# Kernel optimization log

Hardware: AMD Instinct MI355X
Metric: run time of the kernel (lower is better)

## Reference

```python
import jax, jax.numpy as jnp
import numpy as np
import math

B, T, C, H = 2, 2048, 512, 8
TOPK = 64
HD = C // H
EPS = 1e-12  # torch F.normalize eps


def setup_inputs() -> dict:
    key = jax.random.key(0)
    ks = jax.random.split(key, 6)
    s = 1.0 / math.sqrt(C)
    q = jax.random.normal(ks[0], (B, T, C), dtype=jnp.float32)
    tgt_mask = jnp.tril(jnp.ones((T, T), dtype=jnp.float32)).reshape(1, 1, T, T)
    Wq = jax.random.normal(ks[1], (C, C), dtype=jnp.float32) * s
    Wk = jax.random.normal(ks[2], (C, C), dtype=jnp.float32) * s
    Wv = jax.random.normal(ks[3], (C, C), dtype=jnp.float32) * s
    Wp = jax.random.normal(ks[4], (C, C), dtype=jnp.float32) * s
    bq = jnp.zeros((C,), jnp.float32)
    bk = jnp.zeros((C,), jnp.float32)
    bv = jnp.zeros((C,), jnp.float32)
    bp = jnp.zeros((C,), jnp.float32)
    return {"q": q, "tgt_mask": tgt_mask, "Wq": Wq, "bq": bq, "Wk": Wk, "bk": bk,
            "Wv": Wv, "bv": bv, "Wp": Wp, "bp": bp}


def _attn(q, tgt_mask, Wq, bq, Wk, bk, Wv, bv, Wp, bp):
    Bt, Tt, Ct = q.shape
    # self-attention: k = v = q (module path when k, v are None)
    qh = (q @ Wq + bq).reshape(Bt, Tt, H, HD).transpose(0, 2, 1, 3)  # [B,H,T,hd]
    kh = (q @ Wk + bk).reshape(Bt, Tt, H, HD).transpose(0, 2, 1, 3)
    vh = (q @ Wv + bv).reshape(Bt, Tt, H, HD).transpose(0, 2, 1, 3)
    # L2-normalize v along head dim (F.normalize, p=2, eps=1e-12)
    vn = jnp.linalg.norm(vh, axis=-1, keepdims=True)
    vh = vh / jnp.maximum(vn, EPS)
    att = jnp.einsum('bhqd,bhkd->bhqk', qh, kh) * (1.0 / math.sqrt(HD))
    neg = -jnp.inf
    att = jnp.where(tgt_mask[:, :, :Tt, :Tt] == 0, neg, att)
    # top-k sparsification: drop entries strictly below the k-th largest per row
    top = jax.lax.top_k(att, TOPK)[0]            # [B,H,T,TOPK]
    vk = top[..., -1:]                            # k-th largest threshold
    att = jnp.where(att < vk, neg, att)
    att = jax.nn.softmax(att, axis=-1)
    y = jnp.einsum('bhqk,bhkd->bhqd', att, vh)
    y = y.transpose(0, 2, 1, 3).reshape(Bt, Tt, Ct)
    return y @ Wp + bp


def reference(q, tgt_mask, Wq, bq, Wk, bk, Wv, bv, Wp, bp):
    return _attn(q, tgt_mask, Wq, bq, Wk, bk, Wv, bv, Wp, bp)
```

## Files before the change

kernel.cpp:

```cpp
#include <hip/hip_runtime.h>
#include <cstdint>
#include <math.h>

static constexpr int Bc = 2, Tc = 2048, Cch = 512, Hc = 8;
static constexpr int BT = Bc * Tc;
static constexpr int NBH = Bc * Hc;
static constexpr int NRT = Tc / 128;
static constexpr int NTRI = NRT * (NRT + 1) / 2;
static constexpr size_t TRI_FLOATS = (size_t)NTRI * 16384;

typedef float f32x4 __attribute__((ext_vector_type(4)));
typedef short s16x8 __attribute__((ext_vector_type(8)));
typedef unsigned short u16x8 __attribute__((ext_vector_type(8)));
typedef unsigned short u16x4 __attribute__((ext_vector_type(4)));

__device__ __host__ inline constexpr int tri_i(int r) { return r * (r + 1) / 2; }

__device__ inline float wave_sum_f(float x) {
#pragma unroll
  for (int o = 32; o; o >>= 1) x += __shfl_xor(x, o);
  return x;
}
__device__ inline unsigned short f2bf(float x) {
  unsigned u = __float_as_uint(x);
  return (unsigned short)((u + 0x7FFFu + ((u >> 16) & 1u)) >> 16);
}
__device__ inline float bf2f(unsigned short h) { return __uint_as_float(((unsigned)h) << 16); }
__device__ inline float su2f(unsigned s) {
  unsigned u = (s & 0x80000000u) ? (s ^ 0x80000000u) : ~s;
  return __uint_as_float(u);
}

__global__ __launch_bounds__(256) void split_k(const float* __restrict__ X,
    unsigned short* __restrict__ hi, unsigned short* __restrict__ lo, int n8) {
  int i = blockIdx.x * 256 + threadIdx.x;
  if (i >= n8) return;
  const f32x4* p = (const f32x4*)X + (size_t)i * 2;
  f32x4 a = p[0], b = p[1];
  float v[8] = {a[0], a[1], a[2], a[3], b[0], b[1], b[2], b[3]};
  u16x8 h, l;
#pragma unroll
  for (int c = 0; c < 8; c++) {
    unsigned short hh = f2bf(v[c]);
    h[c] = hh;
    l[c] = f2bf(v[c] - bf2f(hh));
  }
  *(u16x8*)(hi + (size_t)i * 8) = h;
  *(u16x8*)(lo + (size_t)i * 8) = l;
}

__global__ __launch_bounds__(256) void splitT_k(const float* __restrict__ W,
    unsigned short* __restrict__ hiT, unsigned short* __restrict__ loT) {
  __shared__ float t[64][65];
  const int tid = threadIdx.x;
  const int k0 = blockIdx.x * 64, n0 = blockIdx.y * 64;
#pragma unroll
  for (int p = 0; p < 4; p++) {
    int idx = tid + p * 256, kk = idx >> 4, n4 = idx & 15;
    f32x4 v = *(const f32x4*)&W[(size_t)(k0 + kk) * Cch + n0 + n4 * 4];
    t[kk][n4 * 4 + 0] = v[0]; t[kk][n4 * 4 + 1] = v[1];
    t[kk][n4 * 4 + 2] = v[2]; t[kk][n4 * 4 + 3] = v[3];
  }
  __syncthreads();
  {
    int n = tid >> 2, ks = tid & 3;
    u16x8 h0, h1, l0, l1;
#pragma unroll
    for (int kk = 0; kk < 8; kk++) {
      float x = t[ks * 16 + kk][n];
      unsigned short hh = f2bf(x);
      h0[kk] = hh; l0[kk] = f2bf(x - bf2f(hh));
      float y = t[ks * 16 + 8 + kk][n];
      unsigned short hy = f2bf(y);
      h1[kk] = hy; l1[kk] = f2bf(y - bf2f(hy));
    }
    size_t base = (size_t)(n0 + n) * Cch + k0 + ks * 16;
    *(u16x8*)(hiT + base) = h0; *(u16x8*)(hiT + base + 8) = h1;
    *(u16x8*)(loT + base) = l0; *(u16x8*)(loT + base + 8) = l1;
  }
}

template <int BF16OUT>
__global__ __launch_bounds__(256) void gemm3_k(
    const unsigned short* __restrict__ Ahi, const unsigned short* __restrict__ Alo,
    const unsigned short* __restrict__ Bhi, const unsigned short* __restrict__ Blo,
    const float* __restrict__ bias, void* __restrict__ Out) {
  __shared__ unsigned short Ah[2][64][72];
  __shared__ unsigned short Bs[2][64][72];
  const int tid = threadIdx.x;
  const int w = tid >> 6, lane = tid & 63, e = lane >> 4, lr = lane & 15;
  const int wr = w >> 1, wc = w & 1;
  const int brow = blockIdx.y * 64, bcol = blockIdx.x * 64;
  f32x4 acc[2][2] = {};
  for (int k0 = 0; k0 < Cch; k0 += 64) {
#pragma unroll
    for (int p = 0; p < 2; p++) {
      int idx = tid + p * 256, row = idx >> 3, seg = idx & 7;
      *(u16x8*)&Ah[0][row][seg * 8] = *(const u16x8*)&Ahi[(size_t)(brow + row) * Cch + k0 + seg * 8];
      *(u16x8*)&Ah[1][row][seg * 8] = *(const u16x8*)&Alo[(size_t)(brow + row) * Cch + k0 + seg * 8];
      *(u16x8*)&Bs[0][row][seg * 8] = *(const u16x8*)&Bhi[(size_t)(bcol + row) * Cch + k0 + seg * 8];
      *(u16x8*)&Bs[1][row][seg * 8] = *(const u16x8*)&Blo[(size_t)(bcol + row) * Cch + k0 + seg * 8];
    }
    __syncthreads();
#pragma unroll
    for (int ks = 0; ks < 2; ks++) {
      s16x8 ah[2], al[2], bh[2], bl[2];
#pragma unroll
      for (int ti = 0; ti < 2; ti++) {
        ah[ti] = *(const s16x8*)&Ah[0][wr * 32 + ti * 16 + lr][ks * 32 + e * 8];
        al[ti] = *(const s16x8*)&Ah[1][wr * 32 + ti * 16 + lr][ks * 32 + e * 8];
      }
#pragma unroll
      for (int tj = 0; tj < 2; tj++) {
        bh[tj] = *(const s16x8*)&Bs[0][wc * 32 + tj * 16 + lr][ks * 32 + e * 8];
        bl[tj] = *(const s16x8*)&Bs[1][wc * 32 + tj * 16 + lr][ks * 32 + e * 8];
      }
#pragma unroll
      for (int ti = 0; ti < 2; ti++)
#pragma unroll
        for (int tj = 0; tj < 2; tj++) {
          acc[ti][tj] = __builtin_amdgcn_mfma_f32_16x16x32_bf16(ah[ti], bh[tj], acc[ti][tj], 0, 0, 0);
          acc[ti][tj] = __builtin_amdgcn_mfma_f32_16x16x32_bf16(ah[ti], bl[tj], acc[ti][tj], 0, 0, 0);
          acc[ti][tj] = __builtin_amdgcn_mfma_f32_16x16x32_bf16(al[ti], bh[tj], acc[ti][tj], 0, 0, 0);
        }
    }
    __syncthreads();
  }
#pragma unroll
  for (int ti = 0; ti < 2; ti++)
#pragma unroll
    for (int tj = 0; tj < 2; tj++) {
      int col = bcol + wc * 32 + tj * 16 + lr;
      float bi = bias[col];
#pragma unroll
      for (int r = 0; r < 4; r++) {
        int row = brow + wr * 32 + ti * 16 + e * 4 + r;
        float v = acc[ti][tj][r] + bi;
        if (BF16OUT) ((unsigned short*)Out)[(size_t)row * Cch + col] = f2bf(v);
        else         ((float*)Out)[(size_t)row * Cch + col] = v;
      }
    }
}

__global__ __launch_bounds__(256) void vnormt_k(const float* __restrict__ Vf,
                                                unsigned short* __restrict__ Vt) {
  __shared__ unsigned short T[64][72];
  const int tid = threadIdx.x;
  const int t0 = blockIdx.x * 64;
  const int h = blockIdx.y;
  const int tok = tid >> 2;
  const int q = tid & 3;
  const float* src = Vf + (size_t)(t0 + tok) * Cch + h * 64 + q * 16;
  f32x4 v[4];
  float ss = 0.f;
#pragma unroll
  for (int i = 0; i < 4; i++) {
    v[i] = *(const f32x4*)(src + i * 4);
#pragma unroll
    for (int c = 0; c < 4; c++) ss += v[i][c] * v[i][c];
  }
  ss += __shfl_xor(ss, 1);
  ss += __shfl_xor(ss, 2);
  float inv = 1.0f / fmaxf(sqrtf(ss), 1e-12f);
#pragma unroll
  for (int i = 0; i < 4; i++)
#pragma unroll
    for (int c = 0; c < 4; c++)
      T[q * 16 + i * 4 + c][tok] = f2bf(v[i][c] * inv);
  __syncthreads();
  const int d = tid >> 2, s2 = (tid & 3) * 2;
  const int b = t0 >> 11;
  size_t base = ((size_t)((b * Hc + h) * 64 + d)) * Tc + (t0 & 2047);
  *(u16x8*)(Vt + base + s2 * 8)     = *(const u16x8*)&T[d][s2 * 8];
  *(u16x8*)(Vt + base + s2 * 8 + 8) = *(const u16x8*)&T[d][s2 * 8 + 8];
}

__global__ __launch_bounds__(512) void sqk_k(const unsigned short* __restrict__ Qp,
    const unsigned short* __restrict__ Kp, float* __restrict__ S, int bh0) {
  __shared__ unsigned short Qs[128][72], Ks[128][72];
  int rt, ct;
  {
    int i = blockIdx.x;
    int r = (int)((sqrtf(8.f * i + 1.f) - 1.f) * 0.5f);
    while ((r + 1) * (r + 2) / 2 <= i) r++;
    while (r * (r + 1) / 2 > i) r--;
    rt = r; ct = i - r * (r + 1) / 2;
  }
  const int bh = bh0 + blockIdx.y, b = bh >> 3, h = bh & 7;
  const int tid = threadIdx.x, w = tid >> 6, lane = tid & 63, e = lane >> 4, lr = lane & 15;
#pragma unroll
  for (int p = 0; p < 2; p++) {
    int idx = tid + p * 512, row = idx >> 3, seg = idx & 7;
    *(u16x8*)&Qs[row][seg * 8] = *(const u16x8*)&Qp[((size_t)(b * Tc + rt * 128 + row)) * Cch + h * 64 + seg * 8];
    *(u16x8*)&Ks[row][seg * 8] = *(const u16x8*)&Kp[((size_t)(b * Tc + ct * 128 + row)) * Cch + h * 64 + seg * 8];
  }
  __syncthreads();
  f32x4 acc[8] = {};
  s16x8 a[2];
#pragma unroll
  for (int ks = 0; ks < 2; ks++) a[ks] = *(const s16x8*)&Qs[w * 16 + lr][ks * 32 + e * 8];
#pragma unroll
  for (int tj = 0; tj < 8; tj++) {
#pragma unroll
    for (int ks = 0; ks < 2; ks++) {
      s16x8 bb = *(const s16x8*)&Ks[tj * 16 + lr][ks * 32 + e * 8];
      acc[tj] = __builtin_amdgcn_mfma_f32_16x16x32_bf16(a[ks], bb, acc[tj], 0, 0, 0);
    }
  }
  float* Srow0 = S + (size_t)(bh - bh0) * TRI_FLOATS + (size_t)tri_i(rt) * 16384;
  const int stride = (rt + 1) * 128;
#pragma unroll
  for (int tj = 0; tj < 8; tj++)
#pragma unroll
    for (int r = 0; r < 4; r++) {
      int row = w * 16 + e * 4 + r;
      Srow0[(size_t)row * stride + ct * 128 + tj * 16 + lr] = acc[tj][r] * 0.125f;
    }
}

__global__ __launch_bounds__(512) void sel_k(float* __restrict__ S) {
  int wid = blockIdx.x * 8 + (threadIdx.x >> 6);
  int lane = threadIdx.x & 63;
  int bhl = wid >> 11, t = wid & 2047;
  int rt = t >> 7, lrow = t & 127;
  int stride = (rt + 1) * 128;
  float* row = S + (size_t)bhl * TRI_FLOATS + (size_t)tri_i(rt) * 16384 + (size_t)lrow * stride;
  unsigned su[32];
#pragma unroll
  for (int c = 0; c < 8; c++) {
    if (c * 256 < stride) {
      int j0 = c * 256 + lane * 4;
      f32x4 v;
      if (j0 < stride) v = *(const f32x4*)(row + j0);
      else { v[0] = v[1] = v[2] = v[3] = -INFINITY; }
#pragma unroll
      for (int cc = 0; cc < 4; cc++) {
        float x = (j0 + cc <= t) ? v[cc] : -INFINITY;
        unsigned u = __float_as_uint(x);
        su[c * 4 + cc] = (u & 0x80000000u) ? ~u : (u | 0x80000000u);
      }
    } else {
#pragma unroll
      for (int cc = 0; cc < 4; cc++) su[c * 4 + cc] = 0x007FFFFFu;
    }
  }
  unsigned lo = 0;
#pragma unroll 1
  for (int bit = 31; bit >= 0; bit--) {
    unsigned cand = lo | (1u << bit);
    int cnt = 0;
#pragma unroll
    for (int c = 0; c < 8; c++)
      if (c * 256 < stride)
#pragma unroll
        for (int q = 0; q < 4; q++)
          cnt += (int)__popcll(__ballot(su[c * 4 + q] >= cand));
    if (cnt >= 64) {
      lo = cand;
      if (cnt == 64) {
        unsigned mn = 0xFFFFFFFFu;
#pragma unroll
        for (int c = 0; c < 8; c++)
          if (c * 256 < stride)
#pragma unroll
            for (int q = 0; q < 4; q++) { unsigned x = (su[c * 4 + q] >= cand) ? su[c * 4 + q] : 0xFFFFFFFFu; mn = mn < x ? mn : x; }
#pragma unroll
        for (int o = 32; o; o >>= 1) { unsigned x = (unsigned)__shfl_xor((int)mn, o); mn = mn < x ? mn : x; }
        lo = mn;
        break;
      }
    }
  }
  unsigned mx = 0;
#pragma unroll
  for (int c = 0; c < 8; c++)
    if (c * 256 < stride)
#pragma unroll
      for (int q = 0; q < 4; q++) mx = mx > su[c * 4 + q] ? mx : su[c * 4 + q];
#pragma unroll
  for (int o = 32; o; o >>= 1) { unsigned x = (unsigned)__shfl_xor((int)mx, o); mx = mx > x ? mx : x; }
  float m = su2f(mx);
  float sum = 0.f;
#pragma unroll
  for (int c = 0; c < 8; c++)
    if (c * 256 < stride)
#pragma unroll
      for (int q = 0; q < 4; q++) {
        float v = su2f(su[c * 4 + q]);
        float wv = (su[c * 4 + q] >= lo) ? __expf(v - m) : 0.f;
        su[c * 4 + q] = __float_as_uint(wv);
        sum += wv;
      }
  sum = wave_sum_f(sum);
  float inv = 1.f / sum;
  unsigned short* prow = (unsigned short*)row;
#pragma unroll
  for (int c = 0; c < 8; c++) {
    if (c * 256 < stride) {
      int j0 = c * 256 + lane * 4;
      if (j0 < stride) {
        u16x4 pk;
#pragma unroll
        for (int cc = 0; cc < 4; cc++) pk[cc] = f2bf(__uint_as_float(su[c * 4 + cc]) * inv);
        *(u16x4*)(prow + j0) = pk;
      }
    }
  }
}

__global__ __launch_bounds__(512) void pv_k(const float* __restrict__ S,
    const unsigned short* __restrict__ Vt,
    unsigned short* __restrict__ Yhi, unsigned short* __restrict__ Ylo, int bh0) {
  __shared__ unsigned short Ps[128][136];
  __shared__ unsigned short Vs[64][136];
  const int rt = blockIdx.x, bh = bh0 + blockIdx.y, b = bh >> 3, h = bh & 7;
  const int tid = threadIdx.x, w = tid >> 6, lane = tid & 63, e = lane >> 4, lr = lane & 15;
  const int stride = (rt + 1) * 128;
  const float* Srow0 = S + (size_t)(bh - bh0) * TRI_FLOATS + (size_t)tri_i(rt) * 16384;
  f32x4 acc[4] = {};
  for (int kt = 0; kt <= rt; kt++) {
#pragma unroll
    for (int p = 0; p < 4; p++) {
      int idx = tid + p * 512, row = idx >> 4, seg = idx & 15;
      const unsigned short* src = (const unsigned short*)(Srow0 + (size_t)row * stride) + kt * 128 + seg * 8;
      *(u16x8*)&Ps[row][seg * 8] = *(const u16x8*)src;
    }
#pragma unroll
    for (int p = 0; p < 2; p++) {
      int idx = tid + p * 512, d = idx >> 4, seg = idx & 15;
      *(u16x8*)&Vs[d][seg * 8] = *(const u16x8*)&Vt[((size_t)(bh * 64 + d)) * Tc + kt * 128 + seg * 8];
    }
    __syncthreads();
#pragma unroll
    for (int ks = 0; ks < 4; ks++) {
      s16x8 a = *(const s16x8*)&Ps[w * 16 + lr][ks * 32 + e * 8];
#pragma unroll
      for (int tj = 0; tj < 4; tj++) {
        s16x8 bb = *(const s16x8*)&Vs[tj * 16 + lr][ks * 32 + e * 8];
        acc[tj] = __builtin_amdgcn_mfma_f32_16x16x32_bf16(a, bb, acc[tj], 0, 0, 0);
      }
    }
    __syncthreads();
  }
#pragma unroll
  for (int tj = 0; tj < 4; tj++)
#pragma unroll
    for (int r = 0; r < 4; r++) {
      int row = rt * 128 + w * 16 + e * 4 + r;
      size_t g = ((size_t)(b * Tc + row)) * Cch + h * 64 + tj * 16 + lr;
      float y = acc[tj][r];
      unsigned short hh = f2bf(y);
      Yhi[g] = hh;
      Ylo[g] = f2bf(y - bf2f(hh));
    }
}

extern "C" void kernel_launch(void* const* d_in, const int* in_sizes, int n_in,
                              void* d_out, int out_size, void* d_ws, size_t ws_size,
                              hipStream_t stream) {
  const float* q  = (const float*)d_in[0];
  const float* Wq = (const float*)d_in[2];
  const float* bq = (const float*)d_in[3];
  const float* Wk = (const float*)d_in[4];
  const float* bk = (const float*)d_in[5];
  const float* Wv = (const float*)d_in[6];
  const float* bv = (const float*)d_in[7];
  const float* Wp = (const float*)d_in[8];
  const float* bp = (const float*)d_in[9];
  float* out = (float*)d_out;
  char* ws = (char*)d_ws;
  constexpr size_t MB = 1u << 20;

  unsigned short* qhi = (unsigned short*)(ws + 0 * MB);
  unsigned short* qlo = (unsigned short*)(ws + 4 * MB);
  unsigned short* Qp  = (unsigned short*)(ws + 8 * MB);
  unsigned short* Kp  = (unsigned short*)(ws + 12 * MB);
  unsigned short* Vt  = (unsigned short*)(ws + 16 * MB);
  unsigned short* wsp = (unsigned short*)(ws + 20 * MB);
  float* Sb = (float*)(ws + 24 * MB);
  float* Vf = (float*)(ws + 24 * MB);
  unsigned short* Yhi = qhi;
  unsigned short* Ylo = qlo;
  auto WT = [&](int i) { return wsp + (size_t)i * 262144; };

  int nbh = NBH;
  while (nbh > 1 && 24 * MB + TRI_FLOATS * 4 * (size_t)nbh > ws_size) nbh >>= 1;

  split_k<<<(BT * Cch / 8 + 255) / 256, 256, 0, stream>>>(q, qhi, qlo, BT * Cch / 8);
  dim3 g8(8, 8);
  splitT_k<<<g8, 256, 0, stream>>>(Wq, WT(0), WT(1));
  splitT_k<<<g8, 256, 0, stream>>>(Wk, WT(2), WT(3));
  splitT_k<<<g8, 256, 0, stream>>>(Wv, WT(4), WT(5));
  splitT_k<<<g8, 256, 0, stream>>>(Wp, WT(6), WT(7));

  dim3 gp(Cch / 64, BT / 64);
  gemm3_k<1><<<gp, 256, 0, stream>>>(qhi, qlo, WT(0), WT(1), bq, Qp);
  gemm3_k<1><<<gp, 256, 0, stream>>>(qhi, qlo, WT(2), WT(3), bk, Kp);
  gemm3_k<0><<<gp, 256, 0, stream>>>(qhi, qlo, WT(4), WT(5), bv, Vf);
  vnormt_k<<<dim3(BT / 64, Hc), 256, 0, stream>>>(Vf, Vt);

  for (int c = 0; c < NBH / nbh; c++) {
    int bh0 = c * nbh;
    sqk_k<<<dim3(NTRI, nbh), 512, 0, stream>>>(Qp, Kp, Sb, bh0);
    sel_k<<<nbh * 256, 512, 0, stream>>>(Sb);
    pv_k<<<dim3(NRT, nbh), 512, 0, stream>>>(Sb, Vt, Yhi, Ylo, bh0);
  }

  gemm3_k<0><<<gp, 256, 0, stream>>>(Yhi, Ylo, WT(6), WT(7), bp, out);
}
```

Measured before the change: 225.8 us.

## Fuse QK scores, top-k select, and PV into one banded attention kernel

```diff
diff --git a/kernel.cpp b/kernel.cpp
--- a/kernel.cpp
+++ b/kernel.cpp
@@ -5,16 +5,13 @@
 static constexpr int Bc = 2, Tc = 2048, Cch = 512, Hc = 8;
 static constexpr int BT = Bc * Tc;
 static constexpr int NBH = Bc * Hc;
-static constexpr int NRT = Tc / 128;
-static constexpr int NTRI = NRT * (NRT + 1) / 2;
-static constexpr size_t TRI_FLOATS = (size_t)NTRI * 16384;
+static constexpr int BANDS = 32;
+static constexpr size_t TRI_FLOATS = 2228224;
 
 typedef float f32x4 __attribute__((ext_vector_type(4)));
 typedef short s16x8 __attribute__((ext_vector_type(8)));
 typedef unsigned short u16x8 __attribute__((ext_vector_type(8)));
 typedef unsigned short u16x4 __attribute__((ext_vector_type(4)));
-
-__device__ __host__ inline constexpr int tri_i(int r) { return r * (r + 1) / 2; }
 
 __device__ inline float wave_sum_f(float x) {
 #pragma unroll
@@ -175,180 +172,187 @@
   *(u16x8*)(Vt + base + s2 * 8 + 8) = *(const u16x8*)&T[d][s2 * 8 + 8];
 }
 
-__global__ __launch_bounds__(512) void sqk_k(const unsigned short* __restrict__ Qp,
-    const unsigned short* __restrict__ Kp, float* __restrict__ S, int bh0) {
-  __shared__ unsigned short Qs[128][72], Ks[128][72];
-  int rt, ct;
+__global__ __launch_bounds__(512, 4) void attn_band_k(
+    const unsigned short* __restrict__ Qp, const unsigned short* __restrict__ Kp,
+    const unsigned short* __restrict__ Vt, float* __restrict__ Sb,
+    unsigned short* __restrict__ Yhi, unsigned short* __restrict__ Ylo, int bh0)
+{
+  __shared__ __align__(16) char smem[35072];
+  unsigned short (*Qs)[72]  = (unsigned short(*)[72])(smem);
+  unsigned short (*Ks)[72]  = (unsigned short(*)[72])(smem + 9216);
+  unsigned short (*Ps)[136] = (unsigned short(*)[136])(smem);
+  unsigned short (*Vs)[136] = (unsigned short(*)[136])(smem + 17408);
+  float* invl = (float*)(smem + 34816);
+
+  const int x = blockIdx.x;
+  const int bb = (x & 1) ? (BANDS - 1 - (x >> 1)) : (x >> 1);
+  const int bh = bh0 + blockIdx.y, b = bh >> 3, h = bh & 7;
+  const int p = bb >> 1;
+  const int stride = (p + 1) * 128;
+  const int nkt = p + 1;
+  float* band = Sb + (size_t)(bh - bh0) * TRI_FLOATS
+              + (size_t)8192 * (size_t)(p + 1) * (size_t)(p + (bb & 1));
+  const int tid = threadIdx.x, w = tid >> 6, lane = tid & 63, e = lane >> 4, lr = lane & 15;
+  const int row0 = bb * 64;
+
   {
-    int i = blockIdx.x;
-    int r = (int)((sqrtf(8.f * i + 1.f) - 1.f) * 0.5f);
-    while ((r + 1) * (r + 2) / 2 <= i) r++;
-    while (r * (r + 1) / 2 > i) r--;
-    rt = r; ct = i - r * (r + 1) / 2;
-  }
-  const int bh = bh0 + blockIdx.y, b = bh >> 3, h = bh & 7;
-  const int tid = threadIdx.x, w = tid >> 6, lane = tid & 63, e = lane >> 4, lr = lane & 15;
-#pragma unroll
-  for (int p = 0; p < 2; p++) {
-    int idx = tid + p * 512, row = idx >> 3, seg = idx & 7;
-    *(u16x8*)&Qs[row][seg * 8] = *(const u16x8*)&Qp[((size_t)(b * Tc + rt * 128 + row)) * Cch + h * 64 + seg * 8];
-    *(u16x8*)&Ks[row][seg * 8] = *(const u16x8*)&Kp[((size_t)(b * Tc + ct * 128 + row)) * Cch + h * 64 + seg * 8];
+    int qr = tid >> 3, seg = tid & 7;
+    *(u16x8*)&Qs[qr][seg * 8] =
+        *(const u16x8*)&Qp[((size_t)(b * Tc + row0 + qr)) * Cch + h * 64 + seg * 8];
   }
   __syncthreads();
-  f32x4 acc[8] = {};
-  s16x8 a[2];
-#pragma unroll
-  for (int ks = 0; ks < 2; ks++) a[ks] = *(const s16x8*)&Qs[w * 16 + lr][ks * 32 + e * 8];
-#pragma unroll
-  for (int tj = 0; tj < 8; tj++) {
+  s16x8 qa[4][2];
+#pragma unroll
+  for (int ti = 0; ti < 4; ti++)
+#pragma unroll
+    for (int ks = 0; ks < 2; ks++)
+      qa[ti][ks] = *(const s16x8*)&Qs[ti * 16 + lr][ks * 32 + e * 8];
+
+  for (int kt = 0; kt < nkt; kt++) {
+#pragma unroll
+    for (int pp = 0; pp < 2; pp++) {
+      int idx = tid + pp * 512, kr = idx >> 3, seg = idx & 7;
+      *(u16x8*)&Ks[kr][seg * 8] =
+          *(const u16x8*)&Kp[((size_t)(b * Tc + kt * 128 + kr)) * Cch + h * 64 + seg * 8];
+    }
+    __syncthreads();
+    f32x4 acc[4] = {};
 #pragma unroll
     for (int ks = 0; ks < 2; ks++) {
-      s16x8 bb = *(const s16x8*)&Ks[tj * 16 + lr][ks * 32 + e * 8];
-      acc[tj] = __builtin_amdgcn_mfma_f32_16x16x32_bf16(a[ks], bb, acc[tj], 0, 0, 0);
-    }
-  }
-  float* Srow0 = S + (size_t)(bh - bh0) * TRI_FLOATS + (size_t)tri_i(rt) * 16384;
-  const int stride = (rt + 1) * 128;
-#pragma unroll
-  for (int tj = 0; tj < 8; tj++)
-#pragma unroll
-    for (int r = 0; r < 4; r++) {
-      int row = w * 16 + e * 4 + r;
-      Srow0[(size_t)row * stride + ct * 128 + tj * 16 + lr] = acc[tj][r] * 0.125f;
-    }
-}
-
-__global__ __launch_bounds__(512) void sel_k(float* __restrict__ S) {
-  int wid = blockIdx.x * 8 + (threadIdx.x >> 6);
-  int lane = threadIdx.x & 63;
-  int bhl = wid >> 11, t = wid & 2047;
-  int rt = t >> 7, lrow = t & 127;
-  int stride = (rt + 1) * 128;
-  float* row = S + (size_t)bhl * TRI_FLOATS + (size_t)tri_i(rt) * 16384 + (size_t)lrow * stride;
-  unsigned su[32];
-#pragma unroll
-  for (int c = 0; c < 8; c++) {
-    if (c * 256 < stride) {
-      int j0 = c * 256 + lane * 4;
-      f32x4 v;
-      if (j0 < stride) v = *(const f32x4*)(row + j0);
-      else { v[0] = v[1] = v[2] = v[3] = -INFINITY; }
-#pragma unroll
-      for (int cc = 0; cc < 4; cc++) {
-        float x = (j0 + cc <= t) ? v[cc] : -INFINITY;
-        unsigned u = __float_as_uint(x);
-        su[c * 4 + cc] = (u & 0x80000000u) ? ~u : (u | 0x80000000u);
-      }
-    } else {
-#pragma unroll
-      for (int cc = 0; cc < 4; cc++) su[c * 4 + cc] = 0x007FFFFFu;
-    }
-  }
-  unsigned lo = 0;
+      s16x8 kb = *(const s16x8*)&Ks[w * 16 + lr][ks * 32 + e * 8];
+#pragma unroll
+      for (int ti = 0; ti < 4; ti++)
+        acc[ti] = __builtin_amdgcn_mfma_f32_16x16x32_bf16(qa[ti][ks], kb, acc[ti], 0, 0, 0);
+    }
+#pragma unroll
+    for (int ti = 0; ti < 4; ti++)
+#pragma unroll
+      for (int r2 = 0; r2 < 4; r2++)
+        band[(size_t)(ti * 16 + e * 4 + r2) * stride + kt * 128 + w * 16 + lr] = acc[ti][r2] * 0.125f;
+    __syncthreads();
+  }
+
 #pragma unroll 1
-  for (int bit = 31; bit >= 0; bit--) {
-    unsigned cand = lo | (1u << bit);
-    int cnt = 0;
+  for (int rr = 0; rr < 8; rr++) {
+    const int lrow = w * 8 + rr;
+    const int t = row0 + lrow;
+    float* row = band + (size_t)lrow * stride;
+    unsigned su[32];
+#pragma unroll
+    for (int c = 0; c < 8; c++) {
+      if (c * 256 < stride) {
+        int j0 = c * 256 + lane * 4;
+        f32x4 v;
+        if (j0 < stride) v = *(const f32x4*)(row + j0);
+        else { v[0] = v[1] = v[2] = v[3] = -INFINITY; }
+#pragma unroll
+        for (int cc = 0; cc < 4; cc++) {
+          float xv = (j0 + cc <= t) ? v[cc] : -INFINITY;
+          unsigned u = __float_as_uint(xv);
+          su[c * 4 + cc] = (u & 0x80000000u) ? ~u : (u | 0x80000000u);
+        }
+      } else {
+#pragma unroll
+        for (int cc = 0; cc < 4; cc++) su[c * 4 + cc] = 0x007FFFFFu;
+      }
+    }
+    unsigned lo = 0;
+#pragma unroll 1
+    for (int bit = 31; bit >= 0; bit--) {
+      unsigned cand = lo | (1u << bit);
+      int cnt = 0;
+#pragma unroll
+      for (int c = 0; c < 8; c++)
+        if (c * 256 < stride)
+#pragma unroll
+          for (int q = 0; q < 4; q++)
+            cnt += (int)__popcll(__ballot(su[c * 4 + q] >= cand));
+      if (cnt >= 64) {
+        lo = cand;
+        if (cnt == 64) {
+          unsigned mn = 0xFFFFFFFFu;
+#pragma unroll
+          for (int c = 0; c < 8; c++)
+            if (c * 256 < stride)
+#pragma unroll
+              for (int q = 0; q < 4; q++) { unsigned xv = (su[c * 4 + q] >= cand) ? su[c * 4 + q] : 0xFFFFFFFFu; mn = mn < xv ? mn : xv; }
+#pragma unroll
+          for (int o = 32; o; o >>= 1) { unsigned xv = (unsigned)__shfl_xor((int)mn, o); mn = mn < xv ? mn : xv; }
+          lo = mn;
+          break;
+        }
+      }
+    }
+    unsigned mx = 0;
 #pragma unroll
     for (int c = 0; c < 8; c++)
       if (c * 256 < stride)
 #pragma unroll
-        for (int q = 0; q < 4; q++)
-          cnt += (int)__popcll(__ballot(su[c * 4 + q] >= cand));
-    if (cnt >= 64) {
-      lo = cand;
-      if (cnt == 64) {
-        unsigned mn = 0xFFFFFFFFu;
-#pragma unroll
-        for (int c = 0; c < 8; c++)
-          if (c * 256 < stride)
-#pragma unroll
-            for (int q = 0; q < 4; q++) { unsigned x = (su[c * 4 + q] >= cand) ? su[c * 4 + q] : 0xFFFFFFFFu; mn = mn < x ? mn : x; }
-#pragma unroll
-        for (int o = 32; o; o >>= 1) { unsigned x = (unsigned)__shfl_xor((int)mn, o); mn = mn < x ? mn : x; }
-        lo = mn;
-        break;
-      }
-    }
-  }
-  unsigned mx = 0;
-#pragma unroll
-  for (int c = 0; c < 8; c++)
-    if (c * 256 < stride)
-#pragma unroll
-      for (int q = 0; q < 4; q++) mx = mx > su[c * 4 + q] ? mx : su[c * 4 + q];
-#pragma unroll
-  for (int o = 32; o; o >>= 1) { unsigned x = (unsigned)__shfl_xor((int)mx, o); mx = mx > x ? mx : x; }
-  float m = su2f(mx);
-  float sum = 0.f;
-#pragma unroll
-  for (int c = 0; c < 8; c++)
-    if (c * 256 < stride)
-#pragma unroll
-      for (int q = 0; q < 4; q++) {
-        float v = su2f(su[c * 4 + q]);
-        float wv = (su[c * 4 + q] >= lo) ? __expf(v - m) : 0.f;
-        su[c * 4 + q] = __float_as_uint(wv);
-        sum += wv;
-      }
-  sum = wave_sum_f(sum);
-  float inv = 1.f / sum;
-  unsigned short* prow = (unsigned short*)row;
-#pragma unroll
-  for (int c = 0; c < 8; c++) {
-    if (c * 256 < stride) {
-      int j0 = c * 256 + lane * 4;
-      if (j0 < stride) {
-        u16x4 pk;
-#pragma unroll
-        for (int cc = 0; cc < 4; cc++) pk[cc] = f2bf(__uint_as_float(su[c * 4 + cc]) * inv);
-        *(u16x4*)(prow + j0) = pk;
-      }
-    }
-  }
-}
-
-__global__ __launch_bounds__(512) void pv_k(const float* __restrict__ S,
-    const unsigned short* __restrict__ Vt,
-    unsigned short* __restrict__ Yhi, unsigned short* __restrict__ Ylo, int bh0) {
-  __shared__ unsigned short Ps[128][136];
-  __shared__ unsigned short Vs[64][136];
-  const int rt = blockIdx.x, bh = bh0 + blockIdx.y, b = bh >> 3, h = bh & 7;
-  const int tid = threadIdx.x, w = tid >> 6, lane = tid & 63, e = lane >> 4, lr = lane & 15;
-  const int stride = (rt + 1) * 128;
-  const float* Srow0 = S + (size_t)(bh - bh0) * TRI_FLOATS + (size_t)tri_i(rt) * 16384;
-  f32x4 acc[4] = {};
-  for (int kt = 0; kt <= rt; kt++) {
-#pragma unroll
-    for (int p = 0; p < 4; p++) {
-      int idx = tid + p * 512, row = idx >> 4, seg = idx & 15;
-      const unsigned short* src = (const unsigned short*)(Srow0 + (size_t)row * stride) + kt * 128 + seg * 8;
-      *(u16x8*)&Ps[row][seg * 8] = *(const u16x8*)src;
-    }
-#pragma unroll
-    for (int p = 0; p < 2; p++) {
-      int idx = tid + p * 512, d = idx >> 4, seg = idx & 15;
-      *(u16x8*)&Vs[d][seg * 8] = *(const u16x8*)&Vt[((size_t)(bh * 64 + d)) * Tc + kt * 128 + seg * 8];
+        for (int q = 0; q < 4; q++) mx = mx > su[c * 4 + q] ? mx : su[c * 4 + q];
+#pragma unroll
+    for (int o = 32; o; o >>= 1) { unsigned xv = (unsigned)__shfl_xor((int)mx, o); mx = mx > xv ? mx : xv; }
+    float m = su2f(mx);
+    float sum = 0.f;
+#pragma unroll
+    for (int c = 0; c < 8; c++)
+      if (c * 256 < stride)
+#pragma unroll
+        for (int q = 0; q < 4; q++) {
+          float v = su2f(su[c * 4 + q]);
+          float wv = (su[c * 4 + q] >= lo) ? __expf(v - m) : 0.f;
+          su[c * 4 + q] = __float_as_uint(wv);
+          sum += wv;
+        }
+    sum = wave_sum_f(sum);
+    if (lane == 0) invl[lrow] = 1.f / sum;
+    unsigned short* prow = (unsigned short*)row;
+#pragma unroll
+    for (int c = 0; c < 8; c++) {
+      if (c * 256 < stride) {
+        int j0 = c * 256 + lane * 4;
+        if (j0 < stride) {
+          u16x4 pk;
+#pragma unroll
+          for (int cc = 0; cc < 4; cc++) pk[cc] = f2bf(__uint_as_float(su[c * 4 + cc]));
+          *(u16x4*)(prow + j0) = pk;
+        }
+      }
+    }
+  }
+  __syncthreads();
+
+  const int ci = w & 3;
+  const int rg = (w >> 2) * 2;
+  f32x4 accp[2] = {};
+  for (int kt = 0; kt < nkt; kt++) {
+#pragma unroll
+    for (int pp = 0; pp < 2; pp++) {
+      int idx = tid + pp * 512, pr = idx >> 4, seg = idx & 15;
+      *(u16x8*)&Ps[pr][seg * 8] =
+          *(const u16x8*)&((const unsigned short*)(band + (size_t)pr * stride))[kt * 128 + seg * 8];
+      int d = pr;
+      *(u16x8*)&Vs[d][seg * 8] =
+          *(const u16x8*)&Vt[((size_t)(bh * 64 + d)) * Tc + kt * 128 + seg * 8];
     }
     __syncthreads();
 #pragma unroll
     for (int ks = 0; ks < 4; ks++) {
-      s16x8 a = *(const s16x8*)&Ps[w * 16 + lr][ks * 32 + e * 8];
-#pragma unroll
-      for (int tj = 0; tj < 4; tj++) {
-        s16x8 bb = *(const s16x8*)&Vs[tj * 16 + lr][ks * 32 + e * 8];
-        acc[tj] = __builtin_amdgcn_mfma_f32_16x16x32_bf16(a, bb, acc[tj], 0, 0, 0);
-      }
-    }
-    __syncthreads();
-  }
-#pragma unroll
-  for (int tj = 0; tj < 4; tj++)
-#pragma unroll
-    for (int r = 0; r < 4; r++) {
-      int row = rt * 128 + w * 16 + e * 4 + r;
-      size_t g = ((size_t)(b * Tc + row)) * Cch + h * 64 + tj * 16 + lr;
-      float y = acc[tj][r];
+      s16x8 bv = *(const s16x8*)&Vs[ci * 16 + lr][ks * 32 + e * 8];
+#pragma unroll
+      for (int tt = 0; tt < 2; tt++) {
+        s16x8 a = *(const s16x8*)&Ps[(rg + tt) * 16 + lr][ks * 32 + e * 8];
+        accp[tt] = __builtin_amdgcn_mfma_f32_16x16x32_bf16(a, bv, accp[tt], 0, 0, 0);
+      }
+    }
+    __syncthreads();
+  }
+#pragma unroll
+  for (int tt = 0; tt < 2; tt++)
+#pragma unroll
+    for (int r2 = 0; r2 < 4; r2++) {
+      int lrow = (rg + tt) * 16 + e * 4 + r2;
+      float y = accp[tt][r2] * invl[lrow];
+      size_t g = ((size_t)(b * Tc + row0 + lrow)) * Cch + h * 64 + ci * 16 + lr;
       unsigned short hh = f2bf(y);
       Yhi[g] = hh;
       Ylo[g] = f2bf(y - bf2f(hh));
@@ -401,9 +405,7 @@
 
   for (int c = 0; c < NBH / nbh; c++) {
     int bh0 = c * nbh;
-    sqk_k<<<dim3(NTRI, nbh), 512, 0, stream>>>(Qp, Kp, Sb, bh0);
-    sel_k<<<nbh * 256, 512, 0, stream>>>(Sb);
-    pv_k<<<dim3(NRT, nbh), 512, 0, stream>>>(Sb, Vt, Yhi, Ylo, bh0);
+    attn_band_k<<<dim3(BANDS, nbh), 512, 0, stream>>>(Qp, Kp, Vt, Sb, Yhi, Ylo, bh0);
   }
 
   gemm3_k<0><<<gp, 256, 0, stream>>>(Yhi, Ylo, WT(6), WT(7), bp, out);
```

After: 280.5 us. +24.2%, slower.
